# Kernel tuning notes

Measured on AMD Instinct MI355X. Metric: run time of the kernel, lower is better.

The kernel has to match this reference:

```python
import jax, jax.numpy as jnp
import numpy as np

B, T, C, H = 8, 2048, 1024, 64


def build_rope_cache(seq_len, dim):
    half = dim // 2
    inv_freq = 1.0 / (10000.0 ** (jnp.arange(half, dtype=jnp.float32) / half))
    t = jnp.arange(seq_len, dtype=jnp.float32)
    freqs = t[:, None] * inv_freq[None, :]          # (T, half)
    cos = jnp.repeat(jnp.cos(freqs), 2, axis=-1)    # (T, dim) interleaved
    sin = jnp.repeat(jnp.sin(freqs), 2, axis=-1)
    return cos, sin


def apply_rope(x, cos, sin):
    # x: (B, T, H); cos/sin: (T, H)
    x1 = x[..., ::2]
    x2 = x[..., 1::2]
    rot = jnp.stack([-x2, x1], axis=-1).reshape(x.shape)
    return x * cos[None] + rot * sin[None]


def setup_inputs() -> dict:
    key = jax.random.key(0)
    kx, kq, kk, kv = jax.random.split(key, 4)
    scale = 1.0 / np.sqrt(C)
    return {
        "x": jax.random.normal(kx, (B, T, C), dtype=jnp.float32),
        "Wq": jax.random.normal(kq, (C, H), dtype=jnp.float32) * scale,
        "Wk": jax.random.normal(kk, (C, H), dtype=jnp.float32) * scale,
        "Wv": jax.random.normal(kv, (C, H), dtype=jnp.float32) * scale,
    }


def reference(x, Wq, Wk, Wv):
    Bc, Tc, _ = x.shape
    head_size = Wq.shape[1]
    cos, sin = build_rope_cache(Tc, head_size)

    q = apply_rope(x @ Wq, cos, sin)   # (B, T, H)
    k = apply_rope(x @ Wk, cos, sin)   # (B, T, H)
    v = x @ Wv                          # (B, T, H)

    # full TxT masked softmax attention (matches original non-fused path)
    wei = jnp.einsum('bth,bsh->bts', q, k) * (head_size ** -0.5)  # (B, T, T)
    causal = jnp.tril(jnp.ones((Tc, Tc), dtype=bool))
    wei = jnp.where(causal[None], wei, -jnp.inf)
    wei = jax.nn.softmax(wei, axis=-1)
    # dropout p=0 (eval mode) -> identity
    return jnp.einsum('bts,bsh->bth', wei, v)
```

## Files before the change

### kernel.cpp

```cpp
#include <hip/hip_runtime.h>
#include <cmath>

#define Tn  2048
#define Cn  1024
#define Hn  64
#define BTn 16384

typedef _Float16 f16x8 __attribute__((ext_vector_type(8)));
typedef _Float16 f16x4 __attribute__((ext_vector_type(4)));
typedef _Float16 f16x2 __attribute__((ext_vector_type(2)));
typedef float    f32x4 __attribute__((ext_vector_type(4)));

#define MFMA16(a, b, c) __builtin_amdgcn_mfma_f32_16x16x32_f16(a, b, c, 0, 0, 0)

__device__ __forceinline__ void gload16(const void* g, void* l) {
    __builtin_amdgcn_global_load_lds(
        (const __attribute__((address_space(1))) void*)g,
        (__attribute__((address_space(3))) void*)l, 16, 0, 0);
}

__global__ __launch_bounds__(256) void prep_w_kernel(
    const float* __restrict__ Wq, const float* __restrict__ Wk,
    const float* __restrict__ Wv, _Float16* __restrict__ Wt)
{
    __shared__ float ts[64][65];
    const int blk = blockIdx.x;
    const int p   = blk >> 4;
    const int c0  = (blk & 15) * 64;
    const float* __restrict__ W = (p == 0) ? Wq : (p == 1) ? Wk : Wv;
    const int tid = threadIdx.x;
    #pragma unroll
    for (int it = 0; it < 16; it++) {
        int idx = tid + it * 256;
        int c = idx >> 6, n = idx & 63;
        ts[c][n] = W[(size_t)(c0 + c) * Hn + n];
    }
    __syncthreads();
    #pragma unroll
    for (int it = 0; it < 16; it++) {
        int idx = tid + it * 256;
        int n = idx >> 6, c = idx & 63;
        Wt[(size_t)(p * 64 + n) * Cn + c0 + c] = (_Float16)ts[c][n];
    }
}

__device__ __forceinline__ f16x8 ldsA(const char* xb, int row, int col) {
    int lb = row * 2048 + col * 4;
    int sw = (row & 7) << 4;
    f32x4 lo = *(const f32x4*)(xb + ((lb     ) ^ sw));
    f32x4 hi = *(const f32x4*)(xb + ((lb + 16) ^ sw));
    f16x8 r;
    r[0] = (_Float16)lo[0]; r[1] = (_Float16)lo[1];
    r[2] = (_Float16)lo[2]; r[3] = (_Float16)lo[3];
    r[4] = (_Float16)hi[0]; r[5] = (_Float16)hi[1];
    r[6] = (_Float16)hi[2]; r[7] = (_Float16)hi[3];
    return r;
}

__global__ __launch_bounds__(512, 4) void proj_kernel(
    const float* __restrict__ x, const _Float16* __restrict__ Wt,
    _Float16* __restrict__ qh, _Float16* __restrict__ kh_out, _Float16* __restrict__ vT)
{
    __shared__ __align__(16) float xsf[32 * 512];
    const int row0 = blockIdx.x * 32;
    const int tid  = threadIdx.x;
    const int wave = tid >> 6, lane = tid & 63;
    const int kh   = wave >> 2;
    const int wc   = wave & 3;
    const int quad = lane >> 4, l15 = lane & 15;

    f32x4 acc[2][3] = {};
    const _Float16* __restrict__ wb = Wt + (size_t)(wc * 48 + l15) * Cn + quad * 8;
    const char* xb = (const char*)xsf;

    #pragma unroll
    for (int ph = 0; ph < 2; ph++) {
        if (ph) __syncthreads();

        {
            const char* xg = (const char*)x + ((size_t)row0 * Cn + ph * 512) * 4;
            char* lb0 = (char*)xsf + wave * 1024;
            #pragma unroll
            for (int r2 = 0; r2 < 8; r2++) {
                int lbl  = tid * 16 + r2 * 8192;
                int row  = lbl >> 11;
                int colb = (lbl & 2047) ^ ((row & 7) << 4);
                gload16(xg + (size_t)row * (Cn * 4) + colb, lb0 + r2 * 8192);
            }
        }
        __syncthreads();

        #pragma unroll
        for (int kc = 0; kc < 8; kc++) {
            const int kf = kh * 256 + kc * 32;
            f16x8 b0 = *(const f16x8*)&wb[ph * 512 + kf];
            f16x8 b1 = *(const f16x8*)&wb[16 * Cn + ph * 512 + kf];
            f16x8 b2 = *(const f16x8*)&wb[32 * Cn + ph * 512 + kf];
            f16x8 a0 = ldsA(xb,      l15, kf + quad * 8);
            f16x8 a1 = ldsA(xb, 16 + l15, kf + quad * 8);
            acc[0][0] = MFMA16(a0, b0, acc[0][0]);
            acc[1][0] = MFMA16(a1, b0, acc[1][0]);
            acc[0][1] = MFMA16(a0, b1, acc[0][1]);
            acc[1][1] = MFMA16(a1, b1, acc[1][1]);
            acc[0][2] = MFMA16(a0, b2, acc[0][2]);
            acc[1][2] = MFMA16(a1, b2, acc[1][2]);
        }
    }

    __syncthreads();
    f32x4* __restrict__ pbuf = (f32x4*)xsf;
    if (kh) {
        #pragma unroll
        for (int mt = 0; mt < 2; mt++)
            #pragma unroll
            for (int nt = 0; nt < 3; nt++)
                pbuf[(mt * 3 + nt) * 256 + wc * 64 + lane] = acc[mt][nt];
    }
    __syncthreads();
    if (kh) return;
    #pragma unroll
    for (int mt = 0; mt < 2; mt++)
        #pragma unroll
        for (int nt = 0; nt < 3; nt++)
            acc[mt][nt] += pbuf[(mt * 3 + nt) * 256 + wc * 64 + lane];

    const int bidx = row0 >> 11;
    #pragma unroll
    for (int nt = 0; nt < 3; nt++) {
        const int n = wc * 48 + nt * 16 + l15;
        const int p = n >> 6;
        const int h = n & 63;
        if (p < 2) {
            _Float16* __restrict__ outb = (p == 0) ? qh : kh_out;
            const float invf = __expf(-0.2878231366242557f * (float)(h >> 1));
            #pragma unroll
            for (int mt = 0; mt < 2; mt++) {
                #pragma unroll
                for (int r = 0; r < 4; r++) {
                    int   row = row0 + mt * 16 + quad * 4 + r;
                    float val = acc[mt][nt][r];
                    float partner = __shfl_xor(val, 1, 64);
                    float ang = (float)(row & (Tn - 1)) * invf;
                    float sv, cv;
                    __sincosf(ang, &sv, &cv);
                    float res = (h & 1) ? fmaf(val, cv,  partner * sv)
                                        : fmaf(val, cv, -partner * sv);
                    if (p == 0) res *= 0.125f;
                    float resn = __shfl_xor(res, 1, 64);
                    if (!(l15 & 1)) {
                        f16x2 pk = { (_Float16)res, (_Float16)resn };
                        *(f16x2*)&outb[(size_t)row * Hn + h] = pk;
                    }
                }
            }
        } else {
            #pragma unroll
            for (int mt = 0; mt < 2; mt++) {
                int t = (row0 & (Tn - 1)) + mt * 16 + quad * 4;
                f16x4 pv = { (_Float16)acc[mt][nt][0], (_Float16)acc[mt][nt][1],
                             (_Float16)acc[mt][nt][2], (_Float16)acc[mt][nt][3] };
                *(f16x4*)&vT[((size_t)bidx * Hn + h) * Tn + t] = pv;
            }
        }
    }
}

#define PSP 72

__global__ __launch_bounds__(256, 4) void attn_kernel(
    const _Float16* __restrict__ qh, const _Float16* __restrict__ kh,
    const _Float16* __restrict__ vT, float* __restrict__ out)
{
    __shared__ _Float16 ps[4][16 * PSP];
    __shared__ float ocomb[4][16][65];
    __shared__ float mlcomb[4][2][16];

    const int blk = blockIdx.x;
    const int b   = blk & 7;
    const int j   = blk >> 3;
    const int jm  = j & 31, g = j >> 5;
    const int qt  = (g == 0) ? (127 - jm)
                  : (g == 1) ? (64 + jm)
                  : (g == 2) ? (63 - jm) : jm;
    const int t0  = qt * 16;
    const int tid = threadIdx.x;
    const int w = tid >> 6, lane = tid & 63;
    const int quad = lane >> 4, l15 = lane & 15;

    const _Float16* __restrict__ qb = qh + (size_t)b * Tn * Hn;
    const _Float16* __restrict__ kb = kh + (size_t)b * Tn * Hn;
    const _Float16* __restrict__ vb = vT + (size_t)b * Hn * Tn;

    const f16x8 aq0 = *(const f16x8*)&qb[(size_t)(t0 + l15) * Hn +      quad * 8];
    const f16x8 aq1 = *(const f16x8*)&qb[(size_t)(t0 + l15) * Hn + 32 + quad * 8];

    float m_run[4], l_run[4];
    f32x4 oacc[4] = {};
    #pragma unroll
    for (int r = 0; r < 4; r++) { m_run[r] = -1e30f; l_run[r] = 0.0f; }

    const int nst = (t0 + 16 + 63) >> 6;
    for (int jt = w; jt < nst; jt += 4) {
        const int s0 = jt * 64;

        f16x8 kf[4][2];
        #pragma unroll
        for (int nt = 0; nt < 4; nt++) {
            const _Float16* kp = &kb[(size_t)(s0 + nt * 16 + l15) * Hn + quad * 8];
            kf[nt][0] = *(const f16x8*)kp;
            kf[nt][1] = *(const f16x8*)(kp + 32);
        }
        f32x4 sacc[4];
        #pragma unroll
        for (int nt = 0; nt < 4; nt++) {
            f32x4 z = {};
            z = MFMA16(aq0, kf[nt][0], z);
            z = MFMA16(aq1, kf[nt][1], z);
            sacc[nt] = z;
        }

        f16x8 vf[2][4];
        #pragma unroll
        for (int sc = 0; sc < 2; sc++)
            #pragma unroll
            for (int ht = 0; ht < 4; ht++)
                vf[sc][ht] = *(const f16x8*)&vb[(size_t)(ht * 16 + l15) * Tn
                                                + s0 + sc * 32 + quad * 8];

        if (jt == nst - 1) {
            #pragma unroll
            for (int nt = 0; nt < 4; nt++)
                #pragma unroll
                for (int r = 0; r < 4; r++) {
                    int scol = s0 + nt * 16 + l15;
                    int trow = t0 + quad * 4 + r;
                    if (scol > trow) sacc[nt][r] = -1e30f;
                }
        }

        float pr[4][4];
        #pragma unroll
        for (int r = 0; r < 4; r++) {
            float mx = fmaxf(fmaxf(sacc[0][r], sacc[1][r]),
                             fmaxf(sacc[2][r], sacc[3][r]));
            #pragma unroll
            for (int off = 1; off < 16; off <<= 1)
                mx = fmaxf(mx, __shfl_xor(mx, off, 64));
            float mnew  = fmaxf(m_run[r], mx);
            float alpha = __expf(m_run[r] - mnew);
            m_run[r] = mnew;
            float rs = 0.0f;
            #pragma unroll
            for (int nt = 0; nt < 4; nt++) {
                float pv = __expf(sacc[nt][r] - mnew);
                pr[nt][r] = pv; rs += pv;
            }
            #pragma unroll
            for (int off = 1; off < 16; off <<= 1)
                rs += __shfl_xor(rs, off, 64);
            l_run[r] = fmaf(l_run[r], alpha, rs);
            #pragma unroll
            for (int ht = 0; ht < 4; ht++)
                oacc[ht][r] = oacc[ht][r] * alpha;
        }

        #pragma unroll
        for (int nt = 0; nt < 4; nt++)
            #pragma unroll
            for (int r = 0; r < 4; r++) {
                float pv = pr[nt][r];
                float pn = __shfl_xor(pv, 1, 64);
                if (!(l15 & 1)) {
                    f16x2 pk = { (_Float16)pv, (_Float16)pn };
                    *(f16x2*)&ps[w][(quad * 4 + r) * PSP + nt * 16 + l15] = pk;
                }
            }

        #pragma unroll
        for (int sc = 0; sc < 2; sc++) {
            f16x8 ap = *(const f16x8*)&ps[w][l15 * PSP + sc * 32 + quad * 8];
            #pragma unroll
            for (int ht = 0; ht < 4; ht++)
                oacc[ht] = MFMA16(ap, vf[sc][ht], oacc[ht]);
        }
    }

    #pragma unroll
    for (int r = 0; r < 4; r++) {
        #pragma unroll
        for (int ht = 0; ht < 4; ht++)
            ocomb[w][quad * 4 + r][ht * 16 + l15] = oacc[ht][r];
        if (l15 == 0) {
            mlcomb[w][0][quad * 4 + r] = m_run[r];
            mlcomb[w][1][quad * 4 + r] = l_run[r];
        }
    }
    __syncthreads();

    #pragma unroll
    for (int rp = 0; rp < 4; rp++) {
        int row = w * 4 + rp;
        float m0 = mlcomb[0][0][row], m1 = mlcomb[1][0][row];
        float m2 = mlcomb[2][0][row], m3 = mlcomb[3][0][row];
        float mm = fmaxf(fmaxf(m0, m1), fmaxf(m2, m3));
        float a0 = __expf(m0 - mm), a1 = __expf(m1 - mm);
        float a2 = __expf(m2 - mm), a3 = __expf(m3 - mm);
        float ll = mlcomb[0][1][row] * a0 + mlcomb[1][1][row] * a1
                 + mlcomb[2][1][row] * a2 + mlcomb[3][1][row] * a3;
        float ov = (ocomb[0][row][lane] * a0 + ocomb[1][row][lane] * a1
                  + ocomb[2][row][lane] * a2 + ocomb[3][row][lane] * a3) / ll;
        out[((size_t)b * Tn + t0 + row) * Hn + lane] = ov;
    }
}

extern "C" void kernel_launch(void* const* d_in, const int* in_sizes, int n_in,
                              void* d_out, int out_size, void* d_ws, size_t ws_size,
                              hipStream_t stream) {
    const float* x  = (const float*)d_in[0];
    const float* Wq = (const float*)d_in[1];
    const float* Wk = (const float*)d_in[2];
    const float* Wv = (const float*)d_in[3];

    const size_t qkvN = (size_t)BTn * Hn;
    _Float16* qh = (_Float16*)d_ws;
    _Float16* kh = qh + qkvN;
    _Float16* vT = kh + qkvN;
    _Float16* Wt = vT + qkvN;

    prep_w_kernel<<<48, 256, 0, stream>>>(Wq, Wk, Wv, Wt);
    proj_kernel<<<BTn / 32, 512, 0, stream>>>(x, Wt, qh, kh, vT);
    attn_kernel<<<1024, 256, 0, stream>>>(qh, kh, vT, (float*)d_out);
}
```

Before: 156.5 us.

## Double-buffer x staging in projection kernel to overlap loads with MFMA

The projection kernel now splits the 1024-wide reduction into four 256-column stages held in two LDS buffers, so the asynchronous global-to-LDS load of the next stage is issued while MFMAs run on the current one. Weight fragments for each stage are prefetched into registers ahead of the stage load, and scheduling barriers fix the instruction order. This targets the exposed global load latency of the old two-phase load-then-compute loop, at the cost of more synchronisation points and higher register pressure from the prefetched weights.

```diff
diff --git a/kernel.cpp b/kernel.cpp
--- a/kernel.cpp
+++ b/kernel.cpp
@@ -45,7 +45,7 @@
 }
 
 __device__ __forceinline__ f16x8 ldsA(const char* xb, int row, int col) {
-    int lb = row * 2048 + col * 4;
+    int lb = row * 1024 + col * 4;
     int sw = (row & 7) << 4;
     f32x4 lo = *(const f32x4*)(xb + ((lb     ) ^ sw));
     f32x4 hi = *(const f32x4*)(xb + ((lb + 16) ^ sw));
@@ -61,7 +61,7 @@
     const float* __restrict__ x, const _Float16* __restrict__ Wt,
     _Float16* __restrict__ qh, _Float16* __restrict__ kh_out, _Float16* __restrict__ vT)
 {
-    __shared__ __align__(16) float xsf[32 * 512];
+    __shared__ __align__(16) float xsf[2][32 * 256];
     const int row0 = blockIdx.x * 32;
     const int tid  = threadIdx.x;
     const int wave = tid >> 6, lane = tid & 63;
@@ -71,43 +71,52 @@
 
     f32x4 acc[2][3] = {};
     const _Float16* __restrict__ wb = Wt + (size_t)(wc * 48 + l15) * Cn + quad * 8;
-    const char* xb = (const char*)xsf;
-
-    #pragma unroll
-    for (int ph = 0; ph < 2; ph++) {
-        if (ph) __syncthreads();
-
-        {
-            const char* xg = (const char*)x + ((size_t)row0 * Cn + ph * 512) * 4;
-            char* lb0 = (char*)xsf + wave * 1024;
-            #pragma unroll
-            for (int r2 = 0; r2 < 8; r2++) {
-                int lbl  = tid * 16 + r2 * 8192;
-                int row  = lbl >> 11;
-                int colb = (lbl & 2047) ^ ((row & 7) << 4);
-                gload16(xg + (size_t)row * (Cn * 4) + colb, lb0 + r2 * 8192);
-            }
+
+    #define STAGE(p)                                                          \
+    {                                                                         \
+        const char* xg = (const char*)(x + (size_t)row0 * Cn + (p) * 256);    \
+        char* lb0 = (char*)xsf[(p) & 1] + wave * 1024;                        \
+        _Pragma("unroll")                                                     \
+        for (int r2 = 0; r2 < 4; r2++) {                                      \
+            int row  = wave + r2 * 8;                                         \
+            int colb = (lane * 16) ^ ((row & 7) << 4);                        \
+            gload16(xg + (size_t)row * (Cn * 4) + colb, lb0 + r2 * 8192);     \
+        }                                                                     \
+    }
+
+    STAGE(0);
+    __syncthreads();
+
+    #pragma unroll
+    for (int p = 0; p < 4; p++) {
+        f16x8 wt[4][3];
+        #pragma unroll
+        for (int kc = 0; kc < 4; kc++) {
+            const int kf = p * 256 + kh * 128 + kc * 32;
+            wt[kc][0] = *(const f16x8*)&wb[kf];
+            wt[kc][1] = *(const f16x8*)&wb[16 * Cn + kf];
+            wt[kc][2] = *(const f16x8*)&wb[32 * Cn + kf];
+        }
+        __builtin_amdgcn_sched_barrier(0);
+        if (p < 3) STAGE(p + 1);
+        __builtin_amdgcn_sched_barrier(0);
+        const char* xb = (const char*)xsf[p & 1];
+        #pragma unroll
+        for (int kc = 0; kc < 4; kc++) {
+            const int cf = kh * 128 + kc * 32 + quad * 8;
+            f16x8 a0 = ldsA(xb,      l15, cf);
+            f16x8 a1 = ldsA(xb, 16 + l15, cf);
+            acc[0][0] = MFMA16(a0, wt[kc][0], acc[0][0]);
+            acc[1][0] = MFMA16(a1, wt[kc][0], acc[1][0]);
+            acc[0][1] = MFMA16(a0, wt[kc][1], acc[0][1]);
+            acc[1][1] = MFMA16(a1, wt[kc][1], acc[1][1]);
+            acc[0][2] = MFMA16(a0, wt[kc][2], acc[0][2]);
+            acc[1][2] = MFMA16(a1, wt[kc][2], acc[1][2]);
         }
         __syncthreads();
-
-        #pragma unroll
-        for (int kc = 0; kc < 8; kc++) {
-            const int kf = kh * 256 + kc * 32;
-            f16x8 b0 = *(const f16x8*)&wb[ph * 512 + kf];
-            f16x8 b1 = *(const f16x8*)&wb[16 * Cn + ph * 512 + kf];
-            f16x8 b2 = *(const f16x8*)&wb[32 * Cn + ph * 512 + kf];
-            f16x8 a0 = ldsA(xb,      l15, kf + quad * 8);
-            f16x8 a1 = ldsA(xb, 16 + l15, kf + quad * 8);
-            acc[0][0] = MFMA16(a0, b0, acc[0][0]);
-            acc[1][0] = MFMA16(a1, b0, acc[1][0]);
-            acc[0][1] = MFMA16(a0, b1, acc[0][1]);
-            acc[1][1] = MFMA16(a1, b1, acc[1][1]);
-            acc[0][2] = MFMA16(a0, b2, acc[0][2]);
-            acc[1][2] = MFMA16(a1, b2, acc[1][2]);
-        }
-    }
-
-    __syncthreads();
+    }
+    #undef STAGE
+
     f32x4* __restrict__ pbuf = (f32x4*)xsf;
     if (kh) {
         #pragma unroll
```

Measured after the change: 154.7 us. About the same (-1.1%).
